# Optimization experiments

Hardware: AMD Instinct MI355X
Metric: run time of the kernel (lower is better)

Reference implementation:

```python
import jax, jax.numpy as jnp
import numpy as np

K = 51  # separable kernel taps
PAD = (K - 1) // 2  # 25


def _lerp_axis(a, n_in, n_out, axis):
    # 1D bilinear resample with align_corners=True semantics
    pos = jnp.arange(n_out, dtype=jnp.float32) * (float(n_in - 1) / float(n_out - 1))
    lo = jnp.floor(pos).astype(jnp.int32)
    hi = jnp.minimum(lo + 1, n_in - 1)
    w = (pos - lo.astype(jnp.float32)).astype(a.dtype)
    shp = [1] * a.ndim
    shp[axis] = n_out
    w = w.reshape(shp)
    return jnp.take(a, lo, axis=axis) * (1 - w) + jnp.take(a, hi, axis=axis) * w


def upsample2x_align_corners(x):
    B, C, H, W = x.shape
    x = _lerp_axis(x, H, 2 * H, 2)
    x = _lerp_axis(x, W, 2 * W, 3)
    return x


def conv3x3(x, w, b):
    y = jax.lax.conv_general_dilated(
        x, w, window_strides=(1, 1), padding=((1, 1), (1, 1)),
        dimension_numbers=('NCHW', 'OIHW', 'NCHW'))
    return y + b[None, :, None, None]


def kernel_block(x, w1, b1, w2, b2, w3, b3):
    h = upsample2x_align_corners(x)
    h = jax.nn.relu(conv3x3(h, w1, b1))
    h = jax.nn.relu(conv3x3(h, w2, b2))
    h = jax.nn.relu(conv3x3(h, w3, b3))
    return h  # [B, 51, H, W]


def sep_conv(img, kv, kh):
    # img: [B,C,H+K-1,W+K-1]; kv, kh: [B,K,H,W]
    # out[b,c,y,x] = sum_{i,j} img[b,c,y+i,x+j] * kv[b,i,y,x] * kh[b,j,y,x]
    B, C, Hp, Wp = img.shape
    H, W = kv.shape[2], kv.shape[3]
    # vertical sliding windows: [B,C,K,H,Wp]
    vwin = jnp.stack([img[:, :, i:i + H, :] for i in range(K)], axis=2)
    out = jnp.zeros((B, C, H, W), img.dtype)
    for j in range(K):  # static loop over K taps
        t = jnp.einsum('bciyx,biyx->bcyx', vwin[:, :, :, :, j:j + W], kv)
        out = out + t * kh[:, j][:, None]
    return out


def setup_inputs() -> dict:
    key = jax.random.key(0)
    ks = jax.random.split(key, 9)
    B, Cf, Hh, Wh = 4, 64, 128, 128  # feature map (half res)
    H, W = 2 * Hh, 2 * Wh
    x = jax.random.normal(ks[0], (B, Cf, Hh, Wh), jnp.float32)
    i1 = jax.random.normal(ks[1], (B, 3, H + 2 * PAD, W + 2 * PAD), jnp.float32)
    i2 = jax.random.normal(ks[2], (B, 3, H + 2 * PAD, W + 2 * PAD), jnp.float32)
    s = 0.05
    W1 = jax.random.normal(ks[3], (4, K, Cf, 3, 3), jnp.float32) * s
    B1 = jax.random.normal(ks[4], (4, K), jnp.float32) * s
    W2 = jax.random.normal(ks[5], (4, K, K, 3, 3), jnp.float32) * s
    B2 = jax.random.normal(ks[6], (4, K), jnp.float32) * s
    W3 = jax.random.normal(ks[7], (4, K, K, 3, 3), jnp.float32) * s
    B3 = jax.random.normal(ks[8], (4, K), jnp.float32) * s
    return {'x': x, 'i1': i1, 'i2': i2,
            'W1': W1, 'B1': B1, 'W2': W2, 'B2': B2, 'W3': W3, 'B3': B3}


def reference(x, i1, i2, W1, B1, W2, B2, W3, B3):
    kernels = [kernel_block(x, W1[k], B1[k], W2[k], B2[k], W3[k], B3[k])
               for k in range(4)]
    k1v, k1h, k2v, k2h = kernels
    y = sep_conv(i1, k1v, k1h) + sep_conv(i2, k2v, k2h)
    return y
```

## Files before the change

kernel.cpp:

```cpp
#include <hip/hip_runtime.h>
#include <stdint.h>

#define HH 128
#define H 256
#define W 256
#define KK 51
#define HIMG 306
#define WIMG 306
#define IMW 312
#define CF 64
#define BB 4
#define HWN (H * W)
#define CHAIN ((size_t)HWN * 64)

typedef short bhalf8 __attribute__((ext_vector_type(8)));
typedef float f32x4 __attribute__((ext_vector_type(4)));

__device__ inline uint16_t f2bf(float f) {
    uint32_t u = __builtin_bit_cast(uint32_t, f);
    u += 0x7FFF + ((u >> 16) & 1);
    return (uint16_t)(u >> 16);
}
__device__ inline float bf2f(uint16_t h) {
    uint32_t u = ((uint32_t)h) << 16;
    return __builtin_bit_cast(float, u);
}

__global__ __launch_bounds__(256) void upsample_cvt(const float* __restrict__ xin,
                                                    uint16_t* __restrict__ upT) {
    __shared__ float SU[2][64][19];
    const int y = blockIdx.x, x0 = blockIdx.y * 32;
    const float s = 127.f / 255.f;
    float py = y * s; int ly = (int)py; int hy = min(ly + 1, 127); float wy = py - (float)ly;
    int lx0 = (int)(x0 * s);
    for (int t = threadIdx.x; t < 2 * 64 * 18; t += 256) {
        int col = t % 18; int c = (t / 18) & 63; int row = t / (18 * 64);
        int sy = row ? hy : ly;
        int sx = min(lx0 + col, 127);
        SU[row][c][col] = xin[((size_t)c * 128 + sy) * 128 + sx];
    }
    __syncthreads();
    const int xl = threadIdx.x & 31, cg = threadIdx.x >> 5;
    const int x = x0 + xl;
    float px = x * s; int lx = (int)px; float wx = px - (float)lx;
    int lxl = lx - lx0;
    int hxl = min(lx + 1, 127) - lx0;
    uint32_t d[4];
#pragma unroll
    for (int q4 = 0; q4 < 4; ++q4) {
        uint32_t two[2];
#pragma unroll
        for (int e = 0; e < 2; ++e) {
            int c = cg * 8 + q4 * 2 + e;
            float v00 = SU[0][c][lxl], v01 = SU[0][c][hxl];
            float v10 = SU[1][c][lxl], v11 = SU[1][c][hxl];
            float a = v00 * (1.f - wy) + v10 * wy;
            float b = v01 * (1.f - wy) + v11 * wy;
            two[e] = f2bf(a * (1.f - wx) + b * wx);
        }
        d[q4] = two[0] | (two[1] << 16);
    }
    uint4 v = {d[0], d[1], d[2], d[3]};
    *(uint4*)(upT + ((size_t)y * W + x) * 64 + cg * 8) = v;
}

__global__ void img_cvt(const float* __restrict__ i1, const float* __restrict__ i2,
                        uint16_t* __restrict__ dst) {
    int task = blockIdx.x * 256 + threadIdx.x;
    if (task >= 7344 * 39) return;
    int ch8 = task % 39, row = task / 39;
    int u0 = ch8 * 8;
    int img = row / 3672;
    int r = row - img * 3672;
    const float* src = (img ? i2 : i1) + (size_t)r * WIMG;
    uint32_t d[4];
#pragma unroll
    for (int p = 0; p < 4; ++p) {
        int u = u0 + p * 2;
        uint32_t lo = (u < WIMG) ? f2bf(src[u]) : 0u;
        uint32_t hi = (u + 1 < WIMG) ? f2bf(src[u + 1]) : 0u;
        d[p] = lo | (hi << 16);
    }
    uint4 v = {d[0], d[1], d[2], d[3]};
    *(uint4*)(dst + (size_t)row * IMW + u0) = v;
}

__global__ void wprep(const float* __restrict__ wsrc, uint16_t* __restrict__ wdst, int cin_act) {
    int g = blockIdx.x * 256 + threadIdx.x;
    if (g >= 4 * 9 * 4 * 2 * 64) return;
    int lane = g & 63;
    int q = g >> 6;
    int ch = q & 1; q >>= 1;
    int m = q & 3; q >>= 2;
    int tap = q % 9;
    int k = q / 9;
    int co = m * 16 + (lane & 15);
    int ci0 = ch * 32 + (lane >> 4) * 8;
    uint32_t d[4];
#pragma unroll
    for (int p = 0; p < 4; ++p) {
        uint32_t w2[2];
#pragma unroll
        for (int e = 0; e < 2; ++e) {
            int ci = ci0 + p * 2 + e;
            float v = 0.f;
            if (co < KK && ci < cin_act)
                v = wsrc[((size_t)(k * KK + co) * cin_act + ci) * 9 + tap];
            w2[e] = f2bf(v);
        }
        d[p] = w2[0] | (w2[1] << 16);
    }
    uint4 v = {d[0], d[1], d[2], d[3]};
    *(uint4*)(wdst + (size_t)g * 8) = v;
}

__global__ __launch_bounds__(256, 2)
void conv_mfma(const uint16_t* __restrict__ in, const uint16_t* __restrict__ wp,
               const float* __restrict__ bias, uint16_t* __restrict__ out,
               size_t in_kstride, int kbase) {
    const int z = blockIdx.z;
    const int k = kbase + z;
    in  += (size_t)z * in_kstride;
    out += (size_t)z * CHAIN;
    const int y0 = blockIdx.x * 4;
    const int x0 = blockIdx.y * 64;
    const int tid = threadIdx.x;
    const int lane = tid & 63;
    const int wv = tid >> 6;
    const int y = y0 + wv;

    __shared__ uint4 lds[6 * 66 * 8];

    uint4 stg[13];
    int   dsti[13];
#pragma unroll
    for (int it = 0; it < 13; ++it) {
        int t = tid + it * 256;
        bool ok = t < 6 * 66 * 8;
        int c = t & 7;
        int q = t >> 3;
        int xl = q % 66;
        int r = q / 66;
        int yg = y0 - 1 + r;
        int xg = x0 + xl - 1;
        uint4 v = {0u, 0u, 0u, 0u};
        if (ok && (unsigned)yg < H && (unsigned)xg < W)
            v = *(const uint4*)(in + (((size_t)yg * W + xg) * 64 + c * 8));
        stg[it] = v;
        dsti[it] = ok ? (q * 8 + (c ^ (xl & 7))) : -1;
    }
#pragma unroll
    for (int it = 0; it < 13; ++it)
        if (dsti[it] >= 0) lds[dsti[it]] = stg[it];
    __syncthreads();

    f32x4 acc[4][4];
#pragma unroll
    for (int m = 0; m < 4; ++m)
#pragma unroll
        for (int n = 0; n < 4; ++n)
            acc[m][n] = (f32x4){0.f, 0.f, 0.f, 0.f};

    const int l4 = lane & 15, g = lane >> 4;
    __builtin_amdgcn_s_setprio(1);
#pragma unroll
    for (int chf = 0; chf < 2; ++chf) {
#pragma unroll
        for (int tap = 0; tap < 9; ++tap) {
            const int ky = tap / 3, kx = tap % 3;
            bhalf8 afr[4];
#pragma unroll
            for (int m = 0; m < 4; ++m)
                afr[m] = *(const bhalf8*)(wp + ((((size_t)(k * 9 + tap) * 4 + m) * 2 + chf) * 64 + lane) * 8);
            const int rrow = wv + ky;
#pragma unroll
            for (int n = 0; n < 4; ++n) {
                int xl = n * 16 + l4 + kx;
                int slot = (chf * 4 + g) ^ (xl & 7);
                bhalf8 bfr = *(const bhalf8*)&lds[((size_t)rrow * 66 + xl) * 8 + slot];
#pragma unroll
                for (int m = 0; m < 4; ++m)
                    acc[m][n] = __builtin_amdgcn_mfma_f32_16x16x32_bf16(afr[m], bfr, acc[m][n], 0, 0, 0);
            }
        }
    }
    __builtin_amdgcn_s_setprio(0);

    __syncthreads();
    const int colx = l4;
    const int r4 = g;
    ushort* ST = (ushort*)lds + wv * 4096;
    float bv[4][4];
#pragma unroll
    for (int m = 0; m < 4; ++m)
#pragma unroll
        for (int r = 0; r < 4; ++r) {
            int co = m * 16 + r4 * 4 + r;
            bv[m][r] = (co < KK) ? bias[k * KK + co] : 0.f;
        }

#pragma unroll
    for (int m = 0; m < 4; ++m) {
#pragma unroll
        for (int nn = 0; nn < 4; ++nn) {
            int xl = nn * 16 + colx;
            uint32_t pk[2];
#pragma unroll
            for (int hh = 0; hh < 2; ++hh) {
                uint32_t lo = f2bf(fmaxf(acc[m][nn][hh * 2]     + bv[m][hh * 2],     0.f));
                uint32_t hi = f2bf(fmaxf(acc[m][nn][hh * 2 + 1] + bv[m][hh * 2 + 1], 0.f));
                pk[hh] = lo | (hi << 16);
            }
            int idx = xl * 64 + ((m * 16 + r4 * 4) ^ ((xl & 7) << 3));
            *(uint2*)(ST + idx) = (uint2){pk[0], pk[1]};
        }
    }
    const int p8 = lane >> 3;
    const int ch = lane & 7;
#pragma unroll
    for (int it = 0; it < 8; ++it) {
        int px = it * 8 + p8;
        uint4 v = *(const uint4*)(ST + px * 64 + ((ch ^ (px & 7)) << 3));
        *(uint4*)(out + (((size_t)y * W + x0 + px) * 64 + ch * 8)) = v;
    }
}

__global__ __launch_bounds__(256, 2)
void sepconv3(const uint16_t* __restrict__ imgb,
              const uint16_t* __restrict__ kvT, const uint16_t* __restrict__ khT,
              float* __restrict__ out, int accum) {
    __shared__ uint4 SB[320 * 8];
    __shared__ float SC[4][16 * 83];
    const int y = blockIdx.x, c = blockIdx.y;
    const int tid = threadIdx.x, lane = tid & 63, wv = tid >> 6;
    const uint16_t* img = imgb + (size_t)c * HIMG * IMW;

    for (int task = tid; task < 40 * 64; task += 256) {
        int i = task & 63;
        int u0 = (task >> 6) * 8;
        uint4 v = {0u, 0u, 0u, 0u};
        if (i <= 50 && u0 < IMW)
            v = *(const uint4*)(img + (size_t)(y + i) * IMW + u0);
        ushort* vs = (ushort*)&v;
#pragma unroll
        for (int e = 0; e < 8; ++e) {
            int u = u0 + e;
            *((ushort*)SB + u * 64 + (((i >> 3) ^ (u & 7)) << 3) + (i & 7)) = vs[e];
        }
    }
    __syncthreads();

    const int l4 = lane & 15, g = lane >> 4;
    for (int xt = 0; xt < 4; ++xt) {
        const int x0 = (wv * 4 + xt) * 16;
        const int xpix = x0 + l4;
        bhalf8 a0 = *(const bhalf8*)(kvT + ((size_t)y * W + xpix) * 64 + g * 8);
        bhalf8 a1 = *(const bhalf8*)(kvT + ((size_t)y * W + xpix) * 64 + 32 + g * 8);
        f32x4 acc[5];
#pragma unroll
        for (int nt = 0; nt < 5; ++nt) acc[nt] = (f32x4){0.f, 0.f, 0.f, 0.f};
#pragma unroll
        for (int nt = 0; nt < 5; ++nt) {
            int u = x0 + nt * 16 + l4;
            bhalf8 b0 = *(const bhalf8*)((ushort*)SB + u * 64 + ((g ^ (u & 7)) << 3));
            acc[nt] = __builtin_amdgcn_mfma_f32_16x16x32_bf16(a0, b0, acc[nt], 0, 0, 0);
            bhalf8 b1 = *(const bhalf8*)((ushort*)SB + u * 64 + (((4 + g) ^ (u & 7)) << 3));
            acc[nt] = __builtin_amdgcn_mfma_f32_16x16x32_bf16(a1, b1, acc[nt], 0, 0, 0);
        }
#pragma unroll
        for (int nt = 0; nt < 5; ++nt)
#pragma unroll
            for (int r = 0; r < 4; ++r)
                SC[wv][(g * 4 + r) * 83 + nt * 16 + l4] = acc[nt][r];

        const uint16_t* khp = khT + ((size_t)y * W + xpix) * 64;
        float partial = 0.f;
#pragma unroll
        for (int jj = 0; jj < 13; ++jj) {
            int j = g * 13 + jj;
            if (j < KK)
                partial = fmaf(SC[wv][l4 * 83 + l4 + j], bf2f(khp[j]), partial);
        }
        partial += __shfl_xor(partial, 16);
        partial += __shfl_xor(partial, 32);
        if (g == 0) {
            size_t oi = ((size_t)c * H + y) * W + xpix;
            if (accum) out[oi] += partial;
            else       out[oi] = partial;
        }
    }
}

extern "C" void kernel_launch(void* const* d_in, const int* in_sizes, int n_in,
                              void* d_out, int out_size, void* d_ws, size_t ws_size,
                              hipStream_t stream) {
    const float* x  = (const float*)d_in[0];
    const float* i1 = (const float*)d_in[1];
    const float* i2 = (const float*)d_in[2];
    const float* W1 = (const float*)d_in[3];
    const float* B1 = (const float*)d_in[4];
    const float* W2 = (const float*)d_in[5];
    const float* B2 = (const float*)d_in[6];
    const float* W3 = (const float*)d_in[7];
    const float* B3 = (const float*)d_in[8];
    float* out = (float*)d_out;

    char* wsb = (char*)d_ws;
    const size_t IMGB = CHAIN * 2;
    const size_t WPN  = 4 * 9 * 4 * 2 * 64 * 8;
    const size_t WPB  = WPN * 2;
    const size_t IMGBYTES = (size_t)2 * 4 * 3 * HIMG * IMW * 2;
    const size_t FULL_NEED = 13 * IMGB + 3 * WPB + IMGBYTES;
    const bool full = ws_size >= FULL_NEED;
    const int IMG_CVT_BLOCKS = (7344 * 39 + 255) / 256;

    if (full) {
        uint16_t* r1   = (uint16_t*)wsb;
        uint16_t* r2   = (uint16_t*)(wsb + 4 * IMGB);
        uint16_t* r3   = (uint16_t*)(wsb + 8 * IMGB);
        uint16_t* upT  = (uint16_t*)(wsb + 12 * IMGB);
        uint16_t* wp1  = (uint16_t*)(wsb + 13 * IMGB);
        uint16_t* wp2  = wp1 + WPN;
        uint16_t* wp3  = wp2 + WPN;
        uint16_t* imgb = wp3 + WPN;

        wprep<<<72, 256, 0, stream>>>(W1, wp1, CF);
        wprep<<<72, 256, 0, stream>>>(W2, wp2, KK);
        wprep<<<72, 256, 0, stream>>>(W3, wp3, KK);
        img_cvt<<<IMG_CVT_BLOCKS, 256, 0, stream>>>(i1, i2, imgb);

        for (int b = 0; b < BB; ++b) {
            upsample_cvt<<<dim3(H, 8), 256, 0, stream>>>(x + (size_t)b * CF * HH * HH, upT);
            conv_mfma<<<dim3(64, 4, 4), 256, 0, stream>>>(upT, wp1, B1, r1, 0, 0);
            conv_mfma<<<dim3(64, 4, 4), 256, 0, stream>>>(r1, wp2, B2, r2, CHAIN, 0);
            conv_mfma<<<dim3(64, 4, 4), 256, 0, stream>>>(r2, wp3, B3, r3, CHAIN, 0);
            for (int p = 0; p < 2; ++p) {
                const uint16_t* ib = imgb + ((size_t)(p * 12 + b * 3) * HIMG) * IMW;
                sepconv3<<<dim3(H, 3), 256, 0, stream>>>(ib,
                        r3 + (size_t)(2 * p) * CHAIN, r3 + (size_t)(2 * p + 1) * CHAIN,
                        out + (size_t)b * 3 * HWN, p);
            }
        }
    } else {
        uint16_t* upT  = (uint16_t*)wsb;
        uint16_t* t1   = (uint16_t*)(wsb + 1 * IMGB);
        uint16_t* t2   = (uint16_t*)(wsb + 3 * IMGB);
        uint16_t* t3   = (uint16_t*)(wsb + 5 * IMGB);
        uint16_t* wp1  = (uint16_t*)(wsb + 7 * IMGB);
        uint16_t* wp2  = wp1 + WPN;
        uint16_t* wp3  = wp2 + WPN;
        uint16_t* imgb = wp3 + WPN;

        wprep<<<72, 256, 0, stream>>>(W1, wp1, CF);
        wprep<<<72, 256, 0, stream>>>(W2, wp2, KK);
        wprep<<<72, 256, 0, stream>>>(W3, wp3, KK);
        img_cvt<<<IMG_CVT_BLOCKS, 256, 0, stream>>>(i1, i2, imgb);

        for (int b = 0; b < BB; ++b) {
            upsample_cvt<<<dim3(H, 8), 256, 0, stream>>>(x + (size_t)b * CF * HH * HH, upT);
            for (int p = 0; p < 2; ++p) {
                conv_mfma<<<dim3(64, 4, 2), 256, 0, stream>>>(upT, wp1, B1, t1, 0, 2 * p);
                conv_mfma<<<dim3(64, 4, 2), 256, 0, stream>>>(t1, wp2, B2, t2, CHAIN, 2 * p);
                conv_mfma<<<dim3(64, 4, 2), 256, 0, stream>>>(t2, wp3, B3, t3, CHAIN, 2 * p);
                const uint16_t* ib = imgb + ((size_t)(p * 12 + b * 3) * HIMG) * IMW;
                sepconv3<<<dim3(H, 3), 256, 0, stream>>>(ib, t3, t3 + CHAIN,
                        out + (size_t)b * 3 * HWN, p);
            }
        }
    }
}
```

Baseline: 595.2 us.

## Stage conv tile via direct global-to-LDS loads and prefetch weight fragments

The 3x3 conv MFMA kernel now loads its input halo tile straight into LDS with global_load_lds instead of staging it through registers. The XOR swizzle moves to the source address, and out-of-bounds entries are zeroed after the wait. Weight fragments are triple-buffered and prefetched two steps ahead of the MFMA loop, and the bias loads are hoisted before the barrier. Launch bounds rise to 3 blocks per CU to raise occupancy, at the cost of tighter register limits that could cause spills.

```diff
diff --git a/kernel.cpp b/kernel.cpp
--- a/kernel.cpp
+++ b/kernel.cpp
@@ -24,6 +24,12 @@
 __device__ inline float bf2f(uint16_t h) {
     uint32_t u = ((uint32_t)h) << 16;
     return __builtin_bit_cast(float, u);
+}
+
+__device__ inline void gload_lds16(const void* g, void* l) {
+    __builtin_amdgcn_global_load_lds(
+        (const __attribute__((address_space(1))) unsigned int*)g,
+        (__attribute__((address_space(3))) unsigned int*)l, 16, 0, 0);
 }
 
 __global__ __launch_bounds__(256) void upsample_cvt(const float* __restrict__ xin,
@@ -114,7 +120,12 @@
     *(uint4*)(wdst + (size_t)g * 8) = v;
 }
 
-__global__ __launch_bounds__(256, 2)
+#define ALOAD(buf, ss) do { const int chf_ = (ss) / 9, tap_ = (ss) % 9;                       \
+    _Pragma("unroll") for (int m_ = 0; m_ < 4; ++m_)                                          \
+        af[buf][m_] = *(const bhalf8*)(wp + ((((size_t)(k * 9 + tap_) * 4 + m_) * 2 + chf_)   \
+                                             * 64 + lane) * 8); } while (0)
+
+__global__ __launch_bounds__(256, 3)
 void conv_mfma(const uint16_t* __restrict__ in, const uint16_t* __restrict__ wp,
                const float* __restrict__ bias, uint16_t* __restrict__ out,
                size_t in_kstride, int kbase) {
@@ -128,30 +139,48 @@
     const int lane = tid & 63;
     const int wv = tid >> 6;
     const int y = y0 + wv;
+    const int l4 = lane & 15, g = lane >> 4;
 
     __shared__ uint4 lds[6 * 66 * 8];
 
-    uint4 stg[13];
-    int   dsti[13];
+    unsigned oobmask = 0;
 #pragma unroll
     for (int it = 0; it < 13; ++it) {
         int t = tid + it * 256;
-        bool ok = t < 6 * 66 * 8;
-        int c = t & 7;
-        int q = t >> 3;
-        int xl = q % 66;
-        int r = q / 66;
-        int yg = y0 - 1 + r;
-        int xg = x0 + xl - 1;
-        uint4 v = {0u, 0u, 0u, 0u};
-        if (ok && (unsigned)yg < H && (unsigned)xg < W)
-            v = *(const uint4*)(in + (((size_t)yg * W + xg) * 64 + c * 8));
-        stg[it] = v;
-        dsti[it] = ok ? (q * 8 + (c ^ (xl & 7))) : -1;
-    }
+        if (t < 6 * 66 * 8) {
+            int c = t & 7;
+            int q = t >> 3;
+            int xl = q % 66;
+            int r = q / 66;
+            int yg = y0 - 1 + r;
+            int xg = x0 + xl - 1;
+            if ((unsigned)yg >= H || (unsigned)xg >= W) {
+                oobmask |= 1u << it;
+                yg = min(max(yg, 0), H - 1);
+                xg = min(max(xg, 0), W - 1);
+            }
+            int cs = c ^ (xl & 7);
+            const uint16_t* src = in + (((size_t)yg * W + xg) * 64 + cs * 8);
+            gload_lds16(src, (char*)lds + ((size_t)it * 256 + wv * 64) * 16);
+        }
+    }
+
+    bhalf8 af[3][4];
+    ALOAD(0, 0);
+    ALOAD(1, 1);
+    float bv[4][4];
+#pragma unroll
+    for (int m = 0; m < 4; ++m)
+#pragma unroll
+        for (int r = 0; r < 4; ++r) {
+            int co = m * 16 + g * 4 + r;
+            bv[m][r] = (co < KK) ? bias[k * KK + co] : 0.f;
+        }
+
+    asm volatile("s_waitcnt vmcnt(0)" ::: "memory");
 #pragma unroll
     for (int it = 0; it < 13; ++it)
-        if (dsti[it] >= 0) lds[dsti[it]] = stg[it];
+        if (oobmask & (1u << it)) lds[tid + it * 256] = (uint4){0u, 0u, 0u, 0u};
     __syncthreads();
 
     f32x4 acc[4][4];
@@ -161,49 +190,32 @@
         for (int n = 0; n < 4; ++n)
             acc[m][n] = (f32x4){0.f, 0.f, 0.f, 0.f};
 
-    const int l4 = lane & 15, g = lane >> 4;
     __builtin_amdgcn_s_setprio(1);
 #pragma unroll
-    for (int chf = 0; chf < 2; ++chf) {
-#pragma unroll
-        for (int tap = 0; tap < 9; ++tap) {
-            const int ky = tap / 3, kx = tap % 3;
-            bhalf8 afr[4];
+    for (int s = 0; s < 18; ++s) {
+        const int chf = s / 9, tap = s % 9;
+        const int ky = tap / 3, kx = tap % 3;
+        if (s + 2 < 18) ALOAD((s + 2) % 3, s + 2);
+        const int rrow = wv + ky;
+#pragma unroll
+        for (int n = 0; n < 4; ++n) {
+            int xl = n * 16 + l4 + kx;
+            int slot = (chf * 4 + g) ^ (xl & 7);
+            bhalf8 bfr = *(const bhalf8*)&lds[((size_t)rrow * 66 + xl) * 8 + slot];
 #pragma unroll
             for (int m = 0; m < 4; ++m)
-                afr[m] = *(const bhalf8*)(wp + ((((size_t)(k * 9 + tap) * 4 + m) * 2 + chf) * 64 + lane) * 8);
-            const int rrow = wv + ky;
-#pragma unroll
-            for (int n = 0; n < 4; ++n) {
-                int xl = n * 16 + l4 + kx;
-                int slot = (chf * 4 + g) ^ (xl & 7);
-                bhalf8 bfr = *(const bhalf8*)&lds[((size_t)rrow * 66 + xl) * 8 + slot];
-#pragma unroll
-                for (int m = 0; m < 4; ++m)
-                    acc[m][n] = __builtin_amdgcn_mfma_f32_16x16x32_bf16(afr[m], bfr, acc[m][n], 0, 0, 0);
-            }
+                acc[m][n] = __builtin_amdgcn_mfma_f32_16x16x32_bf16(af[s % 3][m], bfr, acc[m][n], 0, 0, 0);
         }
     }
     __builtin_amdgcn_s_setprio(0);
 
     __syncthreads();
-    const int colx = l4;
-    const int r4 = g;
     ushort* ST = (ushort*)lds + wv * 4096;
-    float bv[4][4];
-#pragma unroll
-    for (int m = 0; m < 4; ++m)
-#pragma unroll
-        for (int r = 0; r < 4; ++r) {
-            int co = m * 16 + r4 * 4 + r;
-            bv[m][r] = (co < KK) ? bias[k * KK + co] : 0.f;
-        }
-
 #pragma unroll
     for (int m = 0; m < 4; ++m) {
 #pragma unroll
         for (int nn = 0; nn < 4; ++nn) {
-            int xl = nn * 16 + colx;
+            int xl = nn * 16 + l4;
             uint32_t pk[2];
 #pragma unroll
             for (int hh = 0; hh < 2; ++hh) {
@@ -211,7 +223,7 @@
                 uint32_t hi = f2bf(fmaxf(acc[m][nn][hh * 2 + 1] + bv[m][hh * 2 + 1], 0.f));
                 pk[hh] = lo | (hi << 16);
             }
-            int idx = xl * 64 + ((m * 16 + r4 * 4) ^ ((xl & 7) << 3));
+            int idx = xl * 64 + ((m * 16 + g * 4) ^ ((xl & 7) << 3));
             *(uint2*)(ST + idx) = (uint2){pk[0], pk[1]};
         }
     }
```

Measured after the change: 694.2 us. 1.17x slower.

## Batch all images into single launches and fold image conversion into sepconv

Applied to the files above, without the earlier changes.

Adds a batch dimension via blockIdx.z to upsample, conv and sepconv kernels so that, given a large enough workspace, the whole pipeline runs as a few big launches instead of a per-batch loop. This cuts launch count and the tail effects of small grids. The separate img_cvt pass is removed; sepconv now reads fp32 images directly and converts to bf16 while filling LDS. Prepacked weights are staged in the output buffer before it is overwritten, which depends on stream ordering and on the output buffer being large enough.

```diff
diff --git a/kernel.cpp b/kernel.cpp
--- a/kernel.cpp
+++ b/kernel.cpp
@@ -7,7 +7,6 @@
 #define KK 51
 #define HIMG 306
 #define WIMG 306
-#define IMW 312
 #define CF 64
 #define BB 4
 #define HWN (H * W)
@@ -28,6 +27,9 @@
 
 __global__ __launch_bounds__(256) void upsample_cvt(const float* __restrict__ xin,
                                                     uint16_t* __restrict__ upT) {
+    const int z = blockIdx.z;
+    xin += (size_t)z * CF * HH * HH;
+    upT += (size_t)z * CHAIN;
     __shared__ float SU[2][64][19];
     const int y = blockIdx.x, x0 = blockIdx.y * 32;
     const float s = 127.f / 255.f;
@@ -62,27 +64,6 @@
     }
     uint4 v = {d[0], d[1], d[2], d[3]};
     *(uint4*)(upT + ((size_t)y * W + x) * 64 + cg * 8) = v;
-}
-
-__global__ void img_cvt(const float* __restrict__ i1, const float* __restrict__ i2,
-                        uint16_t* __restrict__ dst) {
-    int task = blockIdx.x * 256 + threadIdx.x;
-    if (task >= 7344 * 39) return;
-    int ch8 = task % 39, row = task / 39;
-    int u0 = ch8 * 8;
-    int img = row / 3672;
-    int r = row - img * 3672;
-    const float* src = (img ? i2 : i1) + (size_t)r * WIMG;
-    uint32_t d[4];
-#pragma unroll
-    for (int p = 0; p < 4; ++p) {
-        int u = u0 + p * 2;
-        uint32_t lo = (u < WIMG) ? f2bf(src[u]) : 0u;
-        uint32_t hi = (u + 1 < WIMG) ? f2bf(src[u + 1]) : 0u;
-        d[p] = lo | (hi << 16);
-    }
-    uint4 v = {d[0], d[1], d[2], d[3]};
-    *(uint4*)(dst + (size_t)row * IMW + u0) = v;
 }
 
 __global__ void wprep(const float* __restrict__ wsrc, uint16_t* __restrict__ wdst, int cin_act) {
@@ -117,10 +98,10 @@
 __global__ __launch_bounds__(256, 2)
 void conv_mfma(const uint16_t* __restrict__ in, const uint16_t* __restrict__ wp,
                const float* __restrict__ bias, uint16_t* __restrict__ out,
-               size_t in_kstride, int kbase) {
+               size_t in_cstride, size_t in_bstride, int kbase) {
     const int z = blockIdx.z;
-    const int k = kbase + z;
-    in  += (size_t)z * in_kstride;
+    const int k = kbase + (z & 3);
+    in  += (size_t)(z & 3) * in_cstride + (size_t)(z >> 2) * in_bstride;
     out += (size_t)z * CHAIN;
     const int y0 = blockIdx.x * 4;
     const int x0 = blockIdx.y * 64;
@@ -187,15 +168,13 @@
     __builtin_amdgcn_s_setprio(0);
 
     __syncthreads();
-    const int colx = l4;
-    const int r4 = g;
     ushort* ST = (ushort*)lds + wv * 4096;
     float bv[4][4];
 #pragma unroll
     for (int m = 0; m < 4; ++m)
 #pragma unroll
         for (int r = 0; r < 4; ++r) {
-            int co = m * 16 + r4 * 4 + r;
+            int co = m * 16 + g * 4 + r;
             bv[m][r] = (co < KK) ? bias[k * KK + co] : 0.f;
         }
 
@@ -203,7 +182,7 @@
     for (int m = 0; m < 4; ++m) {
 #pragma unroll
         for (int nn = 0; nn < 4; ++nn) {
-            int xl = nn * 16 + colx;
+            int xl = nn * 16 + l4;
             uint32_t pk[2];
 #pragma unroll
             for (int hh = 0; hh < 2; ++hh) {
@@ -211,7 +190,7 @@
                 uint32_t hi = f2bf(fmaxf(acc[m][nn][hh * 2 + 1] + bv[m][hh * 2 + 1], 0.f));
                 pk[hh] = lo | (hi << 16);
             }
-            int idx = xl * 64 + ((m * 16 + r4 * 4) ^ ((xl & 7) << 3));
+            int idx = xl * 64 + ((m * 16 + g * 4) ^ ((xl & 7) << 3));
             *(uint2*)(ST + idx) = (uint2){pk[0], pk[1]};
         }
     }
@@ -226,26 +205,33 @@
 }
 
 __global__ __launch_bounds__(256, 2)
-void sepconv3(const uint16_t* __restrict__ imgb,
+void sepconv3(const float* __restrict__ img,
               const uint16_t* __restrict__ kvT, const uint16_t* __restrict__ khT,
               float* __restrict__ out, int accum) {
     __shared__ uint4 SB[320 * 8];
     __shared__ float SC[4][16 * 83];
-    const int y = blockIdx.x, c = blockIdx.y;
+    const int y = blockIdx.x, c = blockIdx.y, z = blockIdx.z;
     const int tid = threadIdx.x, lane = tid & 63, wv = tid >> 6;
-    const uint16_t* img = imgb + (size_t)c * HIMG * IMW;
+    const float* ip = img + (size_t)(z * 3 + c) * HIMG * WIMG;
+    kvT += (size_t)z * 4 * CHAIN;
+    khT += (size_t)z * 4 * CHAIN;
 
     for (int task = tid; task < 40 * 64; task += 256) {
         int i = task & 63;
         int u0 = (task >> 6) * 8;
-        uint4 v = {0u, 0u, 0u, 0u};
-        if (i <= 50 && u0 < IMW)
-            v = *(const uint4*)(img + (size_t)(y + i) * IMW + u0);
-        ushort* vs = (ushort*)&v;
+        float f[8];
+        bool rowok = (i <= 50);
+        const float* rp = ip + (size_t)(y + i) * WIMG;
+#pragma unroll
+        for (int e2 = 0; e2 < 4; ++e2) {
+            int u = u0 + e2 * 2;
+            float2 v2 = (rowok && u < WIMG) ? *(const float2*)(rp + u) : float2{0.f, 0.f};
+            f[e2 * 2] = v2.x; f[e2 * 2 + 1] = v2.y;
+        }
 #pragma unroll
         for (int e = 0; e < 8; ++e) {
             int u = u0 + e;
-            *((ushort*)SB + u * 64 + (((i >> 3) ^ (u & 7)) << 3) + (i & 7)) = vs[e];
+            *((ushort*)SB + u * 64 + (((i >> 3) ^ (u & 7)) << 3) + (i & 7)) = f2bf(f[e]);
         }
     }
     __syncthreads();
@@ -284,7 +270,7 @@
         partial += __shfl_xor(partial, 16);
         partial += __shfl_xor(partial, 32);
         if (g == 0) {
-            size_t oi = ((size_t)c * H + y) * W + xpix;
+            size_t oi = ((size_t)(z * 3 + c) * H + y) * W + xpix;
             if (accum) out[oi] += partial;
             else       out[oi] = partial;
         }
@@ -308,62 +294,55 @@
     char* wsb = (char*)d_ws;
     const size_t IMGB = CHAIN * 2;
     const size_t WPN  = 4 * 9 * 4 * 2 * 64 * 8;
-    const size_t WPB  = WPN * 2;
-    const size_t IMGBYTES = (size_t)2 * 4 * 3 * HIMG * IMW * 2;
-    const size_t FULL_NEED = 13 * IMGB + 3 * WPB + IMGBYTES;
-    const bool full = ws_size >= FULL_NEED;
-    const int IMG_CVT_BLOCKS = (7344 * 39 + 255) / 256;
-
-    if (full) {
-        uint16_t* r1   = (uint16_t*)wsb;
-        uint16_t* r2   = (uint16_t*)(wsb + 4 * IMGB);
-        uint16_t* r3   = (uint16_t*)(wsb + 8 * IMGB);
-        uint16_t* upT  = (uint16_t*)(wsb + 12 * IMGB);
-        uint16_t* wp1  = (uint16_t*)(wsb + 13 * IMGB);
-        uint16_t* wp2  = wp1 + WPN;
-        uint16_t* wp3  = wp2 + WPN;
-        uint16_t* imgb = wp3 + WPN;
-
-        wprep<<<72, 256, 0, stream>>>(W1, wp1, CF);
-        wprep<<<72, 256, 0, stream>>>(W2, wp2, KK);
-        wprep<<<72, 256, 0, stream>>>(W3, wp3, KK);
-        img_cvt<<<IMG_CVT_BLOCKS, 256, 0, stream>>>(i1, i2, imgb);
-
+
+    uint16_t* wp1 = (uint16_t*)d_out;
+    uint16_t* wp2 = wp1 + WPN;
+    uint16_t* wp3 = wp2 + WPN;
+    wprep<<<72, 256, 0, stream>>>(W1, wp1, CF);
+    wprep<<<72, 256, 0, stream>>>(W2, wp2, KK);
+    wprep<<<72, 256, 0, stream>>>(W3, wp3, KK);
+
+    if (ws_size >= 32 * IMGB) {
+        uint16_t* A = (uint16_t*)wsb;
+        uint16_t* Bp = (uint16_t*)(wsb + 16 * IMGB);
+        uint16_t* upT = Bp + 12 * CHAIN;
+
+        upsample_cvt<<<dim3(H, 8, BB), 256, 0, stream>>>(x, upT);
+        conv_mfma<<<dim3(64, 4, 16), 256, 0, stream>>>(upT, wp1, B1, A, 0, CHAIN, 0);
+        conv_mfma<<<dim3(64, 4, 16), 256, 0, stream>>>(A,  wp2, B2, Bp, CHAIN, 4 * CHAIN, 0);
+        conv_mfma<<<dim3(64, 4, 16), 256, 0, stream>>>(Bp, wp3, B3, A,  CHAIN, 4 * CHAIN, 0);
+        sepconv3<<<dim3(H, 3, BB), 256, 0, stream>>>(i1, A,             A + CHAIN,     out, 0);
+        sepconv3<<<dim3(H, 3, BB), 256, 0, stream>>>(i2, A + 2 * CHAIN, A + 3 * CHAIN, out, 1);
+    } else if (ws_size >= 13 * IMGB) {
+        uint16_t* r1  = (uint16_t*)wsb;
+        uint16_t* r2  = (uint16_t*)(wsb + 4 * IMGB);
+        uint16_t* r3  = (uint16_t*)(wsb + 8 * IMGB);
+        uint16_t* upT = (uint16_t*)(wsb + 12 * IMGB);
         for (int b = 0; b < BB; ++b) {
-            upsample_cvt<<<dim3(H, 8), 256, 0, stream>>>(x + (size_t)b * CF * HH * HH, upT);
-            conv_mfma<<<dim3(64, 4, 4), 256, 0, stream>>>(upT, wp1, B1, r1, 0, 0);
-            conv_mfma<<<dim3(64, 4, 4), 256, 0, stream>>>(r1, wp2, B2, r2, CHAIN, 0);
-            conv_mfma<<<dim3(64, 4, 4), 256, 0, stream>>>(r2, wp3, B3, r3, CHAIN, 0);
+            upsample_cvt<<<dim3(H, 8, 1), 256, 0, stream>>>(x + (size_t)b * CF * HH * HH, upT);
+            conv_mfma<<<dim3(64, 4, 4), 256, 0, stream>>>(upT, wp1, B1, r1, 0, 0, 0);
+            conv_mfma<<<dim3(64, 4, 4), 256, 0, stream>>>(r1, wp2, B2, r2, CHAIN, 0, 0);
+            conv_mfma<<<dim3(64, 4, 4), 256, 0, stream>>>(r2, wp3, B3, r3, CHAIN, 0, 0);
             for (int p = 0; p < 2; ++p) {
-                const uint16_t* ib = imgb + ((size_t)(p * 12 + b * 3) * HIMG) * IMW;
-                sepconv3<<<dim3(H, 3), 256, 0, stream>>>(ib,
+                const float* img = (p ? i2 : i1) + (size_t)b * 3 * HIMG * WIMG;
+                sepconv3<<<dim3(H, 3, 1), 256, 0, stream>>>(img,
                         r3 + (size_t)(2 * p) * CHAIN, r3 + (size_t)(2 * p + 1) * CHAIN,
                         out + (size_t)b * 3 * HWN, p);
             }
         }
     } else {
-        uint16_t* upT  = (uint16_t*)wsb;
-        uint16_t* t1   = (uint16_t*)(wsb + 1 * IMGB);
-        uint16_t* t2   = (uint16_t*)(wsb + 3 * IMGB);
-        uint16_t* t3   = (uint16_t*)(wsb + 5 * IMGB);
-        uint16_t* wp1  = (uint16_t*)(wsb + 7 * IMGB);
-        uint16_t* wp2  = wp1 + WPN;
-        uint16_t* wp3  = wp2 + WPN;
-        uint16_t* imgb = wp3 + WPN;
-
-        wprep<<<72, 256, 0, stream>>>(W1, wp1, CF);
-        wprep<<<72, 256, 0, stream>>>(W2, wp2, KK);
-        wprep<<<72, 256, 0, stream>>>(W3, wp3, KK);
-        img_cvt<<<IMG_CVT_BLOCKS, 256, 0, stream>>>(i1, i2, imgb);
-
+        uint16_t* upT = (uint16_t*)wsb;
+        uint16_t* t1  = (uint16_t*)(wsb + 1 * IMGB);
+        uint16_t* t2  = (uint16_t*)(wsb + 3 * IMGB);
+        uint16_t* t3  = (uint16_t*)(wsb + 5 * IMGB);
         for (int b = 0; b < BB; ++b) {
-            upsample_cvt<<<dim3(H, 8), 256, 0, stream>>>(x + (size_t)b * CF * HH * HH, upT);
+            upsample_cvt<<<dim3(H, 8, 1), 256, 0, stream>>>(x + (size_t)b * CF * HH * HH, upT);
             for (int p = 0; p < 2; ++p) {
-                conv_mfma<<<dim3(64, 4, 2), 256, 0, stream>>>(upT, wp1, B1, t1, 0, 2 * p);
-                conv_mfma<<<dim3(64, 4, 2), 256, 0, stream>>>(t1, wp2, B2, t2, CHAIN, 2 * p);
-                conv_mfma<<<dim3(64, 4, 2), 256, 0, stream>>>(t2, wp3, B3, t3, CHAIN, 2 * p);
-                const uint16_t* ib = imgb + ((size_t)(p * 12 + b * 3) * HIMG) * IMW;
-                sepconv3<<<dim3(H, 3), 256, 0, stream>>>(ib, t3, t3 + CHAIN,
+                conv_mfma<<<dim3(64, 4, 2), 256, 0, stream>>>(upT, wp1, B1, t1, 0, 0, 2 * p);
+                conv_mfma<<<dim3(64, 4, 2), 256, 0, stream>>>(t1, wp2, B2, t2, CHAIN, 0, 2 * p);
+                conv_mfma<<<dim3(64, 4, 2), 256, 0, stream>>>(t2, wp3, B3, t3, CHAIN, 0, 2 * p);
+                const float* img = (p ? i2 : i1) + (size_t)b * 3 * HIMG * WIMG;
+                sepconv3<<<dim3(H, 3, 1), 256, 0, stream>>>(img, t3, t3 + CHAIN,
                         out + (size_t)b * 3 * HWN, p);
             }
         }
```

Result: faster. 542.4 us (-8.9%).
